# Kernel tuning notes

Measured on AMD Instinct MI355X. Metric: run time of the kernel, lower is better.

The kernel has to match this reference:

```python
import jax, jax.numpy as jnp
import numpy as np

C = 384
HEADS = 8
HEAD_DIM = C // HEADS
BN_EPS = 1e-5


def _bn(x, g, b, m, v):
    # inference-mode BatchNorm2d over channel dim (NCHW)
    inv = jax.lax.rsqrt(v + BN_EPS)
    return (x - m[None, :, None, None]) * (inv * g)[None, :, None, None] + b[None, :, None, None]


def _conv1x1(x, w, b):
    # w: [out, in]; x: [B, in, H, W]
    return jnp.einsum('oc,bchw->bohw', w, x) + b[None, :, None, None]


def setup_inputs() -> dict:
    key = jax.random.key(0)
    ks = jax.random.split(key, 12)
    s = 0.02
    inp = {
        'x': jax.random.normal(ks[0], (16, C, 28, 28), dtype=jnp.float32),
        'local_w': jax.random.normal(ks[1], (C, 1, 3, 3), dtype=jnp.float32) * (1.0 / 3.0),
        'local_b': jnp.zeros((C,), jnp.float32),
        'bn1_g': jnp.ones((C,), jnp.float32),
        'bn1_b': jnp.zeros((C,), jnp.float32),
        'bn1_m': jnp.zeros((C,), jnp.float32),
        'bn1_v': jnp.ones((C,), jnp.float32),
        'q_w': jax.random.normal(ks[2], (C, C), dtype=jnp.float32) * s,
        'q_b': jnp.zeros((C,), jnp.float32),
        'k_w': jax.random.normal(ks[3], (C, C), dtype=jnp.float32) * s,
        'k_b': jnp.zeros((C,), jnp.float32),
        'v_w': jax.random.normal(ks[4], (C, C), dtype=jnp.float32) * s,
        'v_b': jnp.zeros((C,), jnp.float32),
        'proj_w': jax.random.normal(ks[5], (C, C), dtype=jnp.float32) * s,
        'proj_b': jnp.zeros((C,), jnp.float32),
        'ffn1_w': jax.random.normal(ks[6], (4 * C, C), dtype=jnp.float32) * s,
        'ffn1_b': jnp.zeros((4 * C,), jnp.float32),
        'ffn2_w': jax.random.normal(ks[7], (C, 4 * C), dtype=jnp.float32) * s,
        'ffn2_b': jnp.zeros((C,), jnp.float32),
        'bn2_g': jnp.ones((C,), jnp.float32),
        'bn2_b': jnp.zeros((C,), jnp.float32),
        'bn2_m': jnp.zeros((C,), jnp.float32),
        'bn2_v': jnp.ones((C,), jnp.float32),
    }
    return inp


def reference(x, local_w, local_b, bn1_g, bn1_b, bn1_m, bn1_v,
              q_w, q_b, k_w, k_b, v_w, v_b, proj_w, proj_b,
              ffn1_w, ffn1_b, ffn2_w, ffn2_b, bn2_g, bn2_b, bn2_m, bn2_v):
    B, Cc, H, W = x.shape
    N = H * W
    # depthwise 3x3 conv + BN (eval mode)
    lx = jax.lax.conv_general_dilated(
        x, local_w, window_strides=(1, 1), padding='SAME',
        feature_group_count=Cc,
        dimension_numbers=('NCHW', 'OIHW', 'NCHW')) + local_b[None, :, None, None]
    lx = _bn(lx, bn1_g, bn1_b, bn1_m, bn1_v)

    # QKV via 1x1 convs, split into heads over flattened tokens
    q = _conv1x1(lx, q_w, q_b).reshape(B, HEADS, HEAD_DIM, N).transpose(0, 1, 3, 2)  # bhnd
    k = _conv1x1(lx, k_w, k_b).reshape(B, HEADS, HEAD_DIM, N)                          # bhdm
    v = _conv1x1(lx, v_w, v_b).reshape(B, HEADS, HEAD_DIM, N).transpose(0, 1, 3, 2)  # bhmd

    attn = jax.nn.softmax(jnp.einsum('bhnd,bhdm->bhnm', q, k) * (HEAD_DIM ** -0.5), axis=-1)
    out = jnp.einsum('bhnm,bhmd->bhnd', attn, v)
    out = out.transpose(0, 1, 3, 2).reshape(B, Cc, H, W)

    out = _conv1x1(out, proj_w, proj_b) + lx
    residual = out
    h = _bn(out, bn2_g, bn2_b, bn2_m, bn2_v)
    h = _conv1x1(h, ffn1_w, ffn1_b)
    h = jax.nn.gelu(h, approximate=False)
    h = _conv1x1(h, ffn2_w, ffn2_b)
    return h + residual
```

## Files before the change

kernel.cpp:

```cpp
#include <hip/hip_runtime.h>
#include <hip/hip_bf16.h>
#include <math.h>

#define BATCH 16
#define CH 384
#define HH 28
#define WW 28
#define NTOK 784
#define NTOT (BATCH * NTOK)
#define NHEADS 8
#define HDIM 48
#define C4 1536
#define QKVC 1152
#define BN_EPS 1e-5f
#define QTL 128
#define KTL 64
#define WCC (CH * CH)
#define NW_ALL (4 * WCC + 2 * C4 * CH)
#define LAMBDA (0.14433756729740643f * 1.4426950408889634f)
#define VT_BSTRIDE 832
#define VT_CSTRIDE (16 * 832)

typedef __attribute__((ext_vector_type(8))) short bf16x8;
typedef __attribute__((ext_vector_type(4))) float f32x4;

__device__ __forceinline__ void async16(void* lds, const void* g) {
  __builtin_amdgcn_global_load_lds(
      (const __attribute__((address_space(1))) void*)g,
      (__attribute__((address_space(3))) void*)lds, 16, 0, 0);
}
__device__ __forceinline__ float bf2f(__hip_bfloat16 v) { return __bfloat162float(v); }
__device__ __forceinline__ ushort f2bf_bits(float f) {
  __hip_bfloat16 t = __float2bfloat16(f);
  return *reinterpret_cast<ushort*>(&t);
}

__global__ __launch_bounds__(256) void cvt_all(
    const float* __restrict__ q_w, const float* __restrict__ k_w,
    const float* __restrict__ v_w, const float* __restrict__ proj_w,
    const float* __restrict__ ffn1_w, const float* __restrict__ ffn2_w,
    const float* __restrict__ g, const float* __restrict__ vv,
    const float* __restrict__ qb, const float* __restrict__ kb,
    const float* __restrict__ vb, const float* __restrict__ fb1,
    const float* __restrict__ bb2, const float* __restrict__ mm2,
    __hip_bfloat16* __restrict__ wdst, float* __restrict__ qkvb,
    float* __restrict__ fbias, __hip_bfloat16* __restrict__ vtp) {
  int i = blockIdx.x * 256 + threadIdx.x;
  if (i < QKVC) {
    float bvv;
    if (i < CH) bvv = qb[i] * LAMBDA;
    else if (i < 2 * CH) bvv = kb[i - CH];
    else bvv = vb[i - 2 * CH];
    qkvb[i] = bvv;
  }
  if (i < CH * BATCH * 8) {
    const bf16x8 z8 = {0, 0, 0, 0, 0, 0, 0, 0};
    int chunk = i & 7, cb = i >> 3;
    int ch = cb >> 4, b = cb & 15;
    *(bf16x8*)(vtp + (size_t)ch * VT_CSTRIDE + b * VT_BSTRIDE + 768 + chunk * 8) = z8;
  }
  if (i < NW_ALL) {
    float val;
    if (i < WCC) val = q_w[i] * LAMBDA;
    else if (i < 2 * WCC) val = k_w[i - WCC];
    else if (i < 3 * WCC) val = v_w[i - 2 * WCC];
    else if (i < 4 * WCC) val = proj_w[i - 3 * WCC];
    else if (i < 4 * WCC + C4 * CH) {
      int j = i - 4 * WCC;
      int c = j % CH;
      val = ffn1_w[j] * g[c] * rsqrtf(vv[c] + BN_EPS);
    } else {
      val = ffn2_w[i - 4 * WCC - C4 * CH];
    }
    wdst[i] = __float2bfloat16(val);
  }
  if (blockIdx.x < C4 / 4) {
    int w = threadIdx.x >> 6, lane = threadIdx.x & 63;
    int o = blockIdx.x * 4 + w;
    float acc = 0.f;
    for (int c = lane; c < CH; c += 64) {
      float s = g[c] * rsqrtf(vv[c] + BN_EPS);
      acc += ffn1_w[(size_t)o * CH + c] * (bb2[c] - mm2[c] * s);
    }
#pragma unroll
    for (int off = 32; off; off >>= 1) acc += __shfl_xor(acc, off, 64);
    if (lane == 0) fbias[o] = fb1[o] + acc;
  }
}

__global__ __launch_bounds__(256) void dwconv_bn(
    const float* __restrict__ x, const float* __restrict__ w,
    const float* __restrict__ cb, const float* __restrict__ g,
    const float* __restrict__ bnb, const float* __restrict__ m,
    const float* __restrict__ var, __hip_bfloat16* __restrict__ lx) {
  int bc = blockIdx.x;
  int c = bc % CH;
  const float* xp = x + (size_t)bc * NTOK;
  __hip_bfloat16* op = lx + (size_t)bc * NTOK;
  float k[9];
#pragma unroll
  for (int i = 0; i < 9; ++i) k[i] = w[c * 9 + i];
  float s = g[c] * rsqrtf(var[c] + BN_EPS);
  float sh = (cb[c] - m[c]) * s + bnb[c];
  for (int n = threadIdx.x; n < NTOK; n += 256) {
    int y = n / WW, xx = n - y * WW;
    float acc = 0.f;
#pragma unroll
    for (int ky = -1; ky <= 1; ++ky) {
      int yy = y + ky;
      if (yy < 0 || yy >= HH) continue;
#pragma unroll
      for (int kx = -1; kx <= 1; ++kx) {
        int x2 = xx + kx;
        if (x2 < 0 || x2 >= WW) continue;
        acc += k[(ky + 1) * 3 + (kx + 1)] * xp[yy * WW + x2];
      }
    }
    op[n] = __float2bfloat16(acc * s + sh);
  }
}

__global__ __launch_bounds__(256) void transpose_b(
    const ushort* __restrict__ in, ushort* __restrict__ outb) {
  __shared__ ushort t[32][34];
  int b = blockIdx.z, c0 = blockIdx.y * 32, n0 = blockIdx.x * 32;
  int tx = threadIdx.x & 31, ty = threadIdx.x >> 5;
  for (int cc = ty; cc < 32; cc += 8) {
    int n = n0 + tx;
    t[cc][tx] = (n < NTOK) ? in[((size_t)b * CH + c0 + cc) * NTOK + n] : (ushort)0;
  }
  __syncthreads();
  for (int nn = ty; nn < 32; nn += 8) {
    int n = n0 + nn;
    if (n < NTOK) outb[((size_t)b * NTOK + n) * CH + c0 + tx] = t[tx][nn];
  }
}

template <int EPI, int TM, int TN>
__global__ __launch_bounds__(256) void gemm_mfma(
    const __hip_bfloat16* __restrict__ Arows, const __hip_bfloat16* __restrict__ Brows,
    const float* __restrict__ bias, const __hip_bfloat16* __restrict__ resid,
    void* __restrict__ outp, void* __restrict__ outp2, int K) {
  constexpr int NI = TM / 32, NJ = TN / 32;
  __shared__ __align__(16) ushort As[TM * 32];
  __shared__ __align__(16) ushort Bs[TN * 32];
  const int tid = threadIdx.x;
  const int w = tid >> 6;
  const int lane = tid & 63;
  const int quad = lane >> 4;
  const int l16 = lane & 15;
  const int m0 = blockIdx.y * TM;
  const int n0 = blockIdx.x * TN;
  const int wm = (w & 1) * (TM / 2), wn = (w >> 1) * (TN / 2);
  const int NB = gridDim.x * TN;
  const int MB = gridDim.y * TM;

  f32x4 zero = {0.f, 0.f, 0.f, 0.f};
  f32x4 acc[NI][NJ];
#pragma unroll
  for (int i = 0; i < NI; ++i)
#pragma unroll
    for (int j = 0; j < NJ; ++j) acc[i][j] = zero;

  for (int k0 = 0; k0 < K; k0 += 32) {
    __syncthreads();
#pragma unroll
    for (int it = 0; it < (TM * 4 + 255) / 256; ++it) {
      int cbase = it * 256 + w * 64;
      int c = cbase + lane;
      int row = c >> 2;
      int sg = (c & 3) ^ ((c >> 3) & 3);
      async16(As + (size_t)cbase * 8,
              Arows + (size_t)(m0 + row) * K + k0 + sg * 8);
    }
#pragma unroll
    for (int it = 0; it < (TN * 4 + 255) / 256; ++it) {
      int cbase = it * 256 + w * 64;
      int c = cbase + lane;
      int row = c >> 2;
      int sg = (c & 3) ^ ((c >> 3) & 3);
      async16(Bs + (size_t)cbase * 8,
              Brows + (size_t)(n0 + row) * K + k0 + sg * 8);
    }
    __syncthreads();

    bf16x8 af[NI], bf[NJ];
#pragma unroll
    for (int i = 0; i < NI; ++i) {
      int ra = wm + i * 16 + l16;
      int sa = quad ^ ((ra >> 1) & 3);
      af[i] = *(const bf16x8*)&As[ra * 32 + sa * 8];
    }
#pragma unroll
    for (int j = 0; j < NJ; ++j) {
      int rb = wn + j * 16 + l16;
      int sb = quad ^ ((rb >> 1) & 3);
      bf[j] = *(const bf16x8*)&Bs[rb * 32 + sb * 8];
    }
#pragma unroll
    for (int i = 0; i < NI; ++i)
#pragma unroll
      for (int j = 0; j < NJ; ++j)
        acc[i][j] = __builtin_amdgcn_mfma_f32_16x16x32_bf16(af[i], bf[j], acc[i][j], 0, 0, 0);
  }

#pragma unroll
  for (int i = 0; i < NI; ++i) {
#pragma unroll
    for (int j = 0; j < NJ; ++j) {
#pragma unroll
      for (int r = 0; r < 4; ++r) {
        int mrow = m0 + wm + i * 16 + quad * 4 + r;
        int ncol = n0 + wn + j * 16 + l16;
        float val = acc[i][j][r];
        if (EPI == 0) {
          val += bias[ncol];
          if (ncol < 2 * CH) {
            ((__hip_bfloat16*)outp)[(size_t)mrow * (2 * CH) + ncol] = __float2bfloat16(val);
          } else {
            int ch = ncol - 2 * CH;
            int bq = mrow / NTOK;
            int tb = mrow - bq * NTOK;
            int tt = tb & 63, t64 = tb >> 6;
            int phi = ((tt & 15) << 2) | (tt >> 4);
            ((__hip_bfloat16*)outp2)[(size_t)ch * VT_CSTRIDE + bq * VT_BSTRIDE + t64 * 64 + phi] =
                __float2bfloat16(val);
          }
        } else if (EPI <= 2) {
          val += bias[ncol];
          if (EPI == 1) val += bf2f(resid[(size_t)mrow * NB + ncol]);
          if (EPI == 2) val = 0.5f * val * (1.f + erff(val * 0.70710678118654752f));
          ((__hip_bfloat16*)outp)[(size_t)mrow * NB + ncol] = __float2bfloat16(val);
        } else {
          val += bias[mrow];
          val += bf2f(resid[(size_t)ncol * MB + mrow]);
          int bq = ncol / NTOK, nn = ncol - bq * NTOK;
          ((float*)outp)[((size_t)bq * MB + mrow) * NTOK + nn] = val;
        }
      }
    }
  }
}

__global__ __launch_bounds__(256) void attention_mfma2(
    const __hip_bfloat16* __restrict__ qk, const __hip_bfloat16* __restrict__ vt,
    __hip_bfloat16* __restrict__ ob) {
  __shared__ __align__(16) ushort Ks[KTL][72];
  __shared__ __align__(16) ushort Vts[HDIM][72];
  __shared__ __align__(16) ushort Ps[4][32][72];

  const int tid = threadIdx.x;
  const int w = tid >> 6, lane = tid & 63;
  const int quad = lane >> 4, l16 = lane & 15;
  const int h = blockIdx.y, b = blockIdx.z;
  const int n0 = blockIdx.x * QTL;
  const size_t tokbase = (size_t)b * NTOK;
  const bf16x8 z8 = {0, 0, 0, 0, 0, 0, 0, 0};

  bf16x8 aq[2][2];
#pragma unroll
  for (int s = 0; s < 2; ++s) {
    int tok = n0 + w * 32 + s * 16 + l16;
    if (tok >= NTOK) tok = NTOK - 1;
#pragma unroll
    for (int kk = 0; kk < 2; ++kk)
      aq[s][kk] = *(const bf16x8*)(qk + (tokbase + tok) * (2 * CH) + h * HDIM + kk * 32 + quad * 8);
    if (quad >= 2) aq[s][1] = z8;
  }

  bf16x8 kreg[2], vreg[2];
  auto loadK = [&](int m0k) {
#pragma unroll
    for (int t = 0; t < 2; ++t) {
      int c = tid + t * 256;
      int row = c >> 3, hc = c & 7;
      int tok = m0k + row;
      bf16x8 val = z8;
      if (hc < 6 && tok < NTOK)
        val = *(const bf16x8*)(qk + (tokbase + tok) * (2 * CH) + CH + h * HDIM + hc * 8);
      kreg[t] = val;
    }
  };
  auto loadV = [&](int m0k) {
#pragma unroll
    for (int t = 0; t < 2; ++t) {
      int c = tid + t * 256;
      if (c < HDIM * 8) {
        int d = c >> 3, hc = c & 7;
        vreg[t] = *(const bf16x8*)(vt + (size_t)(h * HDIM + d) * VT_CSTRIDE + b * VT_BSTRIDE + m0k + hc * 8);
      }
    }
  };

  float m_i[2][4], l_i[2][4];
#pragma unroll
  for (int s = 0; s < 2; ++s)
#pragma unroll
    for (int r = 0; r < 4; ++r) { m_i[s][r] = -1e30f; l_i[s][r] = 0.f; }
  f32x4 o[2][3];
  const f32x4 zf = {0.f, 0.f, 0.f, 0.f};
#pragma unroll
  for (int s = 0; s < 2; ++s)
#pragma unroll
    for (int t = 0; t < 3; ++t) o[s][t] = zf;

  loadK(0);
  loadV(0);

  for (int m0 = 0; m0 < NTOK; m0 += KTL) {
    __syncthreads();
#pragma unroll
    for (int t = 0; t < 2; ++t) {
      int c = tid + t * 256;
      *(bf16x8*)&Ks[c >> 3][(c & 7) * 8] = kreg[t];
    }
#pragma unroll
    for (int t = 0; t < 2; ++t) {
      int c = tid + t * 256;
      if (c < HDIM * 8) *(bf16x8*)&Vts[c >> 3][(c & 7) * 8] = vreg[t];
    }
    __syncthreads();
    int mn = m0 + KTL;
    if (mn < NTOK) { loadK(mn); loadV(mn); }

    f32x4 sa[2][4];
#pragma unroll
    for (int s = 0; s < 2; ++s)
#pragma unroll
      for (int j = 0; j < 4; ++j) sa[s][j] = zf;
#pragma unroll
    for (int kk = 0; kk < 2; ++kk) {
#pragma unroll
      for (int j = 0; j < 4; ++j) {
        bf16x8 kf = *(const bf16x8*)&Ks[j * 16 + l16][kk * 32 + quad * 8];
        sa[0][j] = __builtin_amdgcn_mfma_f32_16x16x32_bf16(aq[0][kk], kf, sa[0][j], 0, 0, 0);
        sa[1][j] = __builtin_amdgcn_mfma_f32_16x16x32_bf16(aq[1][kk], kf, sa[1][j], 0, 0, 0);
      }
    }

    const bool lastT = (m0 + KTL > NTOK);
    float alpha[2][4];
#pragma unroll
    for (int s = 0; s < 2; ++s) {
#pragma unroll
      for (int r = 0; r < 4; ++r) {
        float sv0 = sa[s][0][r], sv1 = sa[s][1][r], sv2 = sa[s][2][r], sv3 = sa[s][3][r];
        if (lastT) {
          if (m0 + 0 * 16 + l16 >= NTOK) sv0 = -1e30f;
          if (m0 + 1 * 16 + l16 >= NTOK) sv1 = -1e30f;
          if (m0 + 2 * 16 + l16 >= NTOK) sv2 = -1e30f;
          if (m0 + 3 * 16 + l16 >= NTOK) sv3 = -1e30f;
        }
        float mx = fmaxf(fmaxf(sv0, sv1), fmaxf(sv2, sv3));
#pragma unroll
        for (int off = 1; off < 16; off <<= 1) mx = fmaxf(mx, __shfl_xor(mx, off, 16));
        float mnew = fmaxf(m_i[s][r], mx);
        float al = __builtin_amdgcn_exp2f(m_i[s][r] - mnew);
        alpha[s][r] = al;
        m_i[s][r] = mnew;
        float p0 = __builtin_amdgcn_exp2f(sv0 - mnew);
        float p1 = __builtin_amdgcn_exp2f(sv1 - mnew);
        float p2 = __builtin_amdgcn_exp2f(sv2 - mnew);
        float p3 = __builtin_amdgcn_exp2f(sv3 - mnew);
        float sum = (p0 + p1) + (p2 + p3);
        int prow = s * 16 + quad * 4 + r;
        Ps[w][prow][4 * l16 + 0] = f2bf_bits(p0);
        Ps[w][prow][4 * l16 + 1] = f2bf_bits(p1);
        Ps[w][prow][4 * l16 + 2] = f2bf_bits(p2);
        Ps[w][prow][4 * l16 + 3] = f2bf_bits(p3);
#pragma unroll
        for (int off = 1; off < 16; off <<= 1) sum += __shfl_xor(sum, off, 16);
        l_i[s][r] = l_i[s][r] * al + sum;
      }
    }
#pragma unroll
    for (int s = 0; s < 2; ++s)
#pragma unroll
      for (int t = 0; t < 3; ++t)
#pragma unroll
        for (int r = 0; r < 4; ++r) o[s][t][r] *= alpha[s][r];

    __syncthreads();

    bf16x8 pf[2][2];
#pragma unroll
    for (int s = 0; s < 2; ++s)
#pragma unroll
      for (int kk = 0; kk < 2; ++kk)
        pf[s][kk] = *(const bf16x8*)&Ps[w][s * 16 + l16][kk * 32 + quad * 8];
#pragma unroll
    for (int kk = 0; kk < 2; ++kk) {
#pragma unroll
      for (int t = 0; t < 3; ++t) {
        bf16x8 vf = *(const bf16x8*)&Vts[t * 16 + l16][kk * 32 + quad * 8];
        o[0][t] = __builtin_amdgcn_mfma_f32_16x16x32_bf16(pf[0][kk], vf, o[0][t], 0, 0, 0);
        o[1][t] = __builtin_amdgcn_mfma_f32_16x16x32_bf16(pf[1][kk], vf, o[1][t], 0, 0, 0);
      }
    }
  }

#pragma unroll
  for (int s = 0; s < 2; ++s) {
    float inv[4];
#pragma unroll
    for (int r = 0; r < 4; ++r) inv[r] = __builtin_amdgcn_rcpf(l_i[s][r]);
#pragma unroll
    for (int t = 0; t < 3; ++t) {
#pragma unroll
      for (int r = 0; r < 4; ++r) {
        int tok = n0 + w * 32 + s * 16 + quad * 4 + r;
        if (tok < NTOK)
          ob[(tokbase + tok) * CH + h * HDIM + t * 16 + l16] =
              __float2bfloat16(o[s][t][r] * inv[r]);
      }
    }
  }
}

extern "C" void kernel_launch(void* const* d_in, const int* in_sizes, int n_in,
                              void* d_out, int out_size, void* d_ws, size_t ws_size,
                              hipStream_t stream) {
  const float* x       = (const float*)d_in[0];
  const float* local_w = (const float*)d_in[1];
  const float* local_b = (const float*)d_in[2];
  const float* bn1_g   = (const float*)d_in[3];
  const float* bn1_b   = (const float*)d_in[4];
  const float* bn1_m   = (const float*)d_in[5];
  const float* bn1_v   = (const float*)d_in[6];
  const float* q_w     = (const float*)d_in[7];
  const float* q_b     = (const float*)d_in[8];
  const float* k_w     = (const float*)d_in[9];
  const float* k_b     = (const float*)d_in[10];
  const float* v_w     = (const float*)d_in[11];
  const float* v_b     = (const float*)d_in[12];
  const float* proj_w  = (const float*)d_in[13];
  const float* proj_b  = (const float*)d_in[14];
  const float* ffn1_w  = (const float*)d_in[15];
  const float* ffn1_b  = (const float*)d_in[16];
  const float* ffn2_w  = (const float*)d_in[17];
  const float* ffn2_b  = (const float*)d_in[18];
  const float* bn2_g   = (const float*)d_in[19];
  const float* bn2_b   = (const float*)d_in[20];
  const float* bn2_m   = (const float*)d_in[21];
  const float* bn2_v   = (const float*)d_in[22];

  char* wsb = (char*)d_ws;
  __hip_bfloat16* lx_cmb  = (__hip_bfloat16*)(wsb + 0);
  __hip_bfloat16* gelu_a  = (__hip_bfloat16*)(wsb + 0);
  __hip_bfloat16* qk_act  = (__hip_bfloat16*)(wsb + 19267584);
  __hip_bfloat16* attn_a  = (__hip_bfloat16*)(wsb + 48168960);
  __hip_bfloat16* lx_tm   = (__hip_bfloat16*)(wsb + 57802752);
  __hip_bfloat16* resid_a = (__hip_bfloat16*)(wsb + 67436544);
  __hip_bfloat16* w_qkv   = (__hip_bfloat16*)(wsb + 77070336);
  __hip_bfloat16* w_proj  = (__hip_bfloat16*)(wsb + 77955072);
  __hip_bfloat16* w_ffn1  = (__hip_bfloat16*)(wsb + 78249984);
  __hip_bfloat16* w_ffn2  = (__hip_bfloat16*)(wsb + 79429632);
  float*          b_qkv   = (float*)(wsb + 80609280);
  float*          b_ffn1  = (float*)(wsb + 80613888);
  __hip_bfloat16* vt      = (__hip_bfloat16*)(wsb + 85000192);

  cvt_all<<<dim3((NW_ALL + 255) / 256), dim3(256), 0, stream>>>(
      q_w, k_w, v_w, proj_w, ffn1_w, ffn2_w, bn2_g, bn2_v, q_b, k_b, v_b,
      ffn1_b, bn2_b, bn2_m, w_qkv, b_qkv, b_ffn1, vt);

  dwconv_bn<<<dim3(BATCH * CH), dim3(256), 0, stream>>>(
      x, local_w, local_b, bn1_g, bn1_b, bn1_m, bn1_v, lx_cmb);
  transpose_b<<<dim3(25, 12, BATCH), dim3(256), 0, stream>>>(
      (const ushort*)lx_cmb, (ushort*)lx_tm);

  gemm_mfma<0, 128, 128><<<dim3(QKVC / 128, NTOT / 128), dim3(256), 0, stream>>>(
      lx_tm, w_qkv, b_qkv, nullptr, qk_act, vt, CH);

  attention_mfma2<<<dim3((NTOK + QTL - 1) / QTL, NHEADS, BATCH), dim3(256), 0, stream>>>(
      qk_act, vt, attn_a);

  gemm_mfma<1, 128, 64><<<dim3(CH / 64, NTOT / 128), dim3(256), 0, stream>>>(
      attn_a, w_proj, proj_b, lx_tm, resid_a, nullptr, CH);

  gemm_mfma<2, 128, 128><<<dim3(C4 / 128, NTOT / 128), dim3(256), 0, stream>>>(
      resid_a, w_ffn1, b_ffn1, nullptr, gelu_a, nullptr, CH);

  gemm_mfma<3, 64, 128><<<dim3(NTOT / 128, CH / 64), dim3(256), 0, stream>>>(
      w_ffn2, gelu_a, ffn2_b, resid_a, d_out, nullptr, C4);
}
```

Baseline: 365.8 us.

## Fuse prep kernels, deepen GEMM K-step to 64, pack softmax P stores

Merges the weight-conversion and depthwise-conv kernels into one launch, removing a kernel boundary. The GEMM now loads 64-wide K slices per barrier pair instead of 32, halving synchronisation count at the cost of doubled LDS per block. The attention kernel packs pairs of bf16 probabilities into 32-bit LDS stores, cutting store instruction count. These are three unrelated changes bundled together.

```diff
diff --git a/kernel.cpp b/kernel.cpp
--- a/kernel.cpp
+++ b/kernel.cpp
@@ -23,6 +23,7 @@
 
 typedef __attribute__((ext_vector_type(8))) short bf16x8;
 typedef __attribute__((ext_vector_type(4))) float f32x4;
+typedef __attribute__((ext_vector_type(4))) uint uint4v;
 
 __device__ __forceinline__ void async16(void* lds, const void* g) {
   __builtin_amdgcn_global_load_lds(
@@ -30,22 +31,55 @@
       (__attribute__((address_space(3))) void*)lds, 16, 0, 0);
 }
 __device__ __forceinline__ float bf2f(__hip_bfloat16 v) { return __bfloat162float(v); }
-__device__ __forceinline__ ushort f2bf_bits(float f) {
+__device__ __forceinline__ uint f2bf_bits(float f) {
   __hip_bfloat16 t = __float2bfloat16(f);
-  return *reinterpret_cast<ushort*>(&t);
-}
-
-__global__ __launch_bounds__(256) void cvt_all(
+  return (uint)*reinterpret_cast<ushort*>(&t);
+}
+
+__global__ __launch_bounds__(256) void prep_fused(
+    const float* __restrict__ x, const float* __restrict__ lw,
+    const float* __restrict__ lb, const float* __restrict__ g1,
+    const float* __restrict__ b1, const float* __restrict__ m1,
+    const float* __restrict__ v1, __hip_bfloat16* __restrict__ lx,
     const float* __restrict__ q_w, const float* __restrict__ k_w,
     const float* __restrict__ v_w, const float* __restrict__ proj_w,
     const float* __restrict__ ffn1_w, const float* __restrict__ ffn2_w,
-    const float* __restrict__ g, const float* __restrict__ vv,
+    const float* __restrict__ g2, const float* __restrict__ vv2,
     const float* __restrict__ qb, const float* __restrict__ kb,
     const float* __restrict__ vb, const float* __restrict__ fb1,
     const float* __restrict__ bb2, const float* __restrict__ mm2,
     __hip_bfloat16* __restrict__ wdst, float* __restrict__ qkvb,
     float* __restrict__ fbias, __hip_bfloat16* __restrict__ vtp) {
-  int i = blockIdx.x * 256 + threadIdx.x;
+  int bid = blockIdx.x;
+  if (bid < BATCH * CH) {
+    int c = bid % CH;
+    const float* xp = x + (size_t)bid * NTOK;
+    __hip_bfloat16* op = lx + (size_t)bid * NTOK;
+    float k[9];
+#pragma unroll
+    for (int i = 0; i < 9; ++i) k[i] = lw[c * 9 + i];
+    float s = g1[c] * rsqrtf(v1[c] + BN_EPS);
+    float sh = (lb[c] - m1[c]) * s + b1[c];
+    for (int n = threadIdx.x; n < NTOK; n += 256) {
+      int y = n / WW, xx = n - y * WW;
+      float acc = 0.f;
+#pragma unroll
+      for (int ky = -1; ky <= 1; ++ky) {
+        int yy = y + ky;
+        if (yy < 0 || yy >= HH) continue;
+#pragma unroll
+        for (int kx = -1; kx <= 1; ++kx) {
+          int x2 = xx + kx;
+          if (x2 < 0 || x2 >= WW) continue;
+          acc += k[(ky + 1) * 3 + (kx + 1)] * xp[yy * WW + x2];
+        }
+      }
+      op[n] = __float2bfloat16(acc * s + sh);
+    }
+    return;
+  }
+  int cb = bid - BATCH * CH;
+  int i = cb * 256 + threadIdx.x;
   if (i < QKVC) {
     float bvv;
     if (i < CH) bvv = qb[i] * LAMBDA;
@@ -55,8 +89,8 @@
   }
   if (i < CH * BATCH * 8) {
     const bf16x8 z8 = {0, 0, 0, 0, 0, 0, 0, 0};
-    int chunk = i & 7, cb = i >> 3;
-    int ch = cb >> 4, b = cb & 15;
+    int chunk = i & 7, cb2 = i >> 3;
+    int ch = cb2 >> 4, b = cb2 & 15;
     *(bf16x8*)(vtp + (size_t)ch * VT_CSTRIDE + b * VT_BSTRIDE + 768 + chunk * 8) = z8;
   }
   if (i < NW_ALL) {
@@ -68,55 +102,23 @@
     else if (i < 4 * WCC + C4 * CH) {
       int j = i - 4 * WCC;
       int c = j % CH;
-      val = ffn1_w[j] * g[c] * rsqrtf(vv[c] + BN_EPS);
+      val = ffn1_w[j] * g2[c] * rsqrtf(vv2[c] + BN_EPS);
     } else {
       val = ffn2_w[i - 4 * WCC - C4 * CH];
     }
     wdst[i] = __float2bfloat16(val);
   }
-  if (blockIdx.x < C4 / 4) {
+  if (cb < C4 / 4) {
     int w = threadIdx.x >> 6, lane = threadIdx.x & 63;
-    int o = blockIdx.x * 4 + w;
+    int o = cb * 4 + w;
     float acc = 0.f;
     for (int c = lane; c < CH; c += 64) {
-      float s = g[c] * rsqrtf(vv[c] + BN_EPS);
+      float s = g2[c] * rsqrtf(vv2[c] + BN_EPS);
       acc += ffn1_w[(size_t)o * CH + c] * (bb2[c] - mm2[c] * s);
     }
 #pragma unroll
     for (int off = 32; off; off >>= 1) acc += __shfl_xor(acc, off, 64);
     if (lane == 0) fbias[o] = fb1[o] + acc;
-  }
-}
-
-__global__ __launch_bounds__(256) void dwconv_bn(
-    const float* __restrict__ x, const float* __restrict__ w,
-    const float* __restrict__ cb, const float* __restrict__ g,
-    const float* __restrict__ bnb, const float* __restrict__ m,
-    const float* __restrict__ var, __hip_bfloat16* __restrict__ lx) {
-  int bc = blockIdx.x;
-  int c = bc % CH;
-  const float* xp = x + (size_t)bc * NTOK;
-  __hip_bfloat16* op = lx + (size_t)bc * NTOK;
-  float k[9];
-#pragma unroll
-  for (int i = 0; i < 9; ++i) k[i] = w[c * 9 + i];
-  float s = g[c] * rsqrtf(var[c] + BN_EPS);
-  float sh = (cb[c] - m[c]) * s + bnb[c];
-  for (int n = threadIdx.x; n < NTOK; n += 256) {
-    int y = n / WW, xx = n - y * WW;
-    float acc = 0.f;
-#pragma unroll
-    for (int ky = -1; ky <= 1; ++ky) {
-      int yy = y + ky;
-      if (yy < 0 || yy >= HH) continue;
-#pragma unroll
-      for (int kx = -1; kx <= 1; ++kx) {
-        int x2 = xx + kx;
-        if (x2 < 0 || x2 >= WW) continue;
-        acc += k[(ky + 1) * 3 + (kx + 1)] * xp[yy * WW + x2];
-      }
-    }
-    op[n] = __float2bfloat16(acc * s + sh);
   }
 }
 
@@ -142,8 +144,8 @@
     const float* __restrict__ bias, const __hip_bfloat16* __restrict__ resid,
     void* __restrict__ outp, void* __restrict__ outp2, int K) {
   constexpr int NI = TM / 32, NJ = TN / 32;
-  __shared__ __align__(16) ushort As[TM * 32];
-  __shared__ __align__(16) ushort Bs[TN * 32];
+  __shared__ __align__(16) ushort As[2 * TM * 32];
+  __shared__ __align__(16) ushort Bs[2 * TN * 32];
   const int tid = threadIdx.x;
   const int w = tid >> 6;
   const int lane = tid & 63;
@@ -162,46 +164,53 @@
 #pragma unroll
     for (int j = 0; j < NJ; ++j) acc[i][j] = zero;
 
-  for (int k0 = 0; k0 < K; k0 += 32) {
+  for (int k0 = 0; k0 < K; k0 += 64) {
     __syncthreads();
 #pragma unroll
-    for (int it = 0; it < (TM * 4 + 255) / 256; ++it) {
+    for (int it = 0; it < TM * 8 / 256; ++it) {
       int cbase = it * 256 + w * 64;
       int c = cbase + lane;
-      int row = c >> 2;
-      int sg = (c & 3) ^ ((c >> 3) & 3);
+      int kh = c / (TM * 4);
+      int rem = c - kh * (TM * 4);
+      int row = rem >> 2;
+      int sg = (rem & 3) ^ ((row >> 1) & 3);
       async16(As + (size_t)cbase * 8,
-              Arows + (size_t)(m0 + row) * K + k0 + sg * 8);
-    }
-#pragma unroll
-    for (int it = 0; it < (TN * 4 + 255) / 256; ++it) {
+              Arows + (size_t)(m0 + row) * K + k0 + kh * 32 + sg * 8);
+    }
+#pragma unroll
+    for (int it = 0; it < TN * 8 / 256; ++it) {
       int cbase = it * 256 + w * 64;
       int c = cbase + lane;
-      int row = c >> 2;
-      int sg = (c & 3) ^ ((c >> 3) & 3);
+      int kh = c / (TN * 4);
+      int rem = c - kh * (TN * 4);
+      int row = rem >> 2;
+      int sg = (rem & 3) ^ ((row >> 1) & 3);
       async16(Bs + (size_t)cbase * 8,
-              Brows + (size_t)(n0 + row) * K + k0 + sg * 8);
+              Brows + (size_t)(n0 + row) * K + k0 + kh * 32 + sg * 8);
     }
     __syncthreads();
 
-    bf16x8 af[NI], bf[NJ];
-#pragma unroll
-    for (int i = 0; i < NI; ++i) {
-      int ra = wm + i * 16 + l16;
-      int sa = quad ^ ((ra >> 1) & 3);
-      af[i] = *(const bf16x8*)&As[ra * 32 + sa * 8];
-    }
-#pragma unroll
-    for (int j = 0; j < NJ; ++j) {
-      int rb = wn + j * 16 + l16;
-      int sb = quad ^ ((rb >> 1) & 3);
-      bf[j] = *(const bf16x8*)&Bs[rb * 32 + sb * 8];
-    }
-#pragma unroll
-    for (int i = 0; i < NI; ++i)
-#pragma unroll
-      for (int j = 0; j < NJ; ++j)
-        acc[i][j] = __builtin_amdgcn_mfma_f32_16x16x32_bf16(af[i], bf[j], acc[i][j], 0, 0, 0);
+#pragma unroll
+    for (int kk = 0; kk < 2; ++kk) {
+      bf16x8 af[NI], bf[NJ];
+#pragma unroll
+      for (int i = 0; i < NI; ++i) {
+        int ra = wm + i * 16 + l16;
+        int sa = quad ^ ((ra >> 1) & 3);
+        af[i] = *(const bf16x8*)&As[(kk * TM * 4 + ra * 4 + sa) * 8];
+      }
+#pragma unroll
+      for (int j = 0; j < NJ; ++j) {
+        int rb = wn + j * 16 + l16;
+        int sb = quad ^ ((rb >> 1) & 3);
+        bf[j] = *(const bf16x8*)&Bs[(kk * TN * 4 + rb * 4 + sb) * 8];
+      }
+#pragma unroll
+      for (int i = 0; i < NI; ++i)
+#pragma unroll
+        for (int j = 0; j < NJ; ++j)
+          acc[i][j] = __builtin_amdgcn_mfma_f32_16x16x32_bf16(af[i], bf[j], acc[i][j], 0, 0, 0);
+    }
   }
 
 #pragma unroll
@@ -247,7 +256,7 @@
     __hip_bfloat16* __restrict__ ob) {
   __shared__ __align__(16) ushort Ks[KTL][72];
   __shared__ __align__(16) ushort Vts[HDIM][72];
-  __shared__ __align__(16) ushort Ps[4][32][72];
+  __shared__ __align__(16) uint Ps[4][32][36];
 
   const int tid = threadIdx.x;
   const int w = tid >> 6, lane = tid & 63;
@@ -364,10 +373,8 @@
         float p3 = __builtin_amdgcn_exp2f(sv3 - mnew);
         float sum = (p0 + p1) + (p2 + p3);
         int prow = s * 16 + quad * 4 + r;
-        Ps[w][prow][4 * l16 + 0] = f2bf_bits(p0);
-        Ps[w][prow][4 * l16 + 1] = f2bf_bits(p1);
-        Ps[w][prow][4 * l16 + 2] = f2bf_bits(p2);
-        Ps[w][prow][4 * l16 + 3] = f2bf_bits(p3);
+        Ps[w][prow][l16 * 2 + 0] = f2bf_bits(p0) | (f2bf_bits(p1) << 16);
+        Ps[w][prow][l16 * 2 + 1] = f2bf_bits(p2) | (f2bf_bits(p3) << 16);
 #pragma unroll
         for (int off = 1; off < 16; off <<= 1) sum += __shfl_xor(sum, off, 16);
         l_i[s][r] = l_i[s][r] * al + sum;
@@ -386,8 +393,10 @@
 #pragma unroll
     for (int s = 0; s < 2; ++s)
 #pragma unroll
-      for (int kk = 0; kk < 2; ++kk)
-        pf[s][kk] = *(const bf16x8*)&Ps[w][s * 16 + l16][kk * 32 + quad * 8];
+      for (int kk = 0; kk < 2; ++kk) {
+        uint4v u = *(const uint4v*)&Ps[w][s * 16 + l16][kk * 16 + quad * 4];
+        pf[s][kk] = __builtin_bit_cast(bf16x8, u);
+      }
 #pragma unroll
     for (int kk = 0; kk < 2; ++kk) {
 #pragma unroll
@@ -459,12 +468,12 @@
   float*          b_ffn1  = (float*)(wsb + 80613888);
   __hip_bfloat16* vt      = (__hip_bfloat16*)(wsb + 85000192);
 
-  cvt_all<<<dim3((NW_ALL + 255) / 256), dim3(256), 0, stream>>>(
-      q_w, k_w, v_w, proj_w, ffn1_w, ffn2_w, bn2_g, bn2_v, q_b, k_b, v_b,
-      ffn1_b, bn2_b, bn2_m, w_qkv, b_qkv, b_ffn1, vt);
-
-  dwconv_bn<<<dim3(BATCH * CH), dim3(256), 0, stream>>>(
-      x, local_w, local_b, bn1_g, bn1_b, bn1_m, bn1_v, lx_cmb);
+  const int CVT_BLOCKS = (NW_ALL + 255) / 256;
+  prep_fused<<<dim3(BATCH * CH + CVT_BLOCKS), dim3(256), 0, stream>>>(
+      x, local_w, local_b, bn1_g, bn1_b, bn1_m, bn1_v, lx_cmb,
+      q_w, k_w, v_w, proj_w, ffn1_w, ffn2_w, bn2_g, bn2_v,
+      q_b, k_b, v_b, ffn1_b, bn2_b, bn2_m, w_qkv, b_qkv, b_ffn1, vt);
+
   transpose_b<<<dim3(25, 12, BATCH), dim3(256), 0, stream>>>(
       (const ushort*)lx_cmb, (ushort*)lx_tm);
 
```

Measured after the change: 368.7 us. No clear change (+0.8%).
